# Performance work log

Hardware: AMD Instinct MI355X
Metric: run time of the kernel (lower is better)

The kernel has to match this reference:

```python
import jax, jax.numpy as jnp
import numpy as np

N_HEAD = 16
D_K = 64
D_V = 64
EMBED = 1024
BATCH = 4
SEQ = 2048

def setup_inputs() -> dict:
    key = jax.random.key(0)
    ks = jax.random.split(key, 12)
    s = lambda d: 1.0 / np.sqrt(d)
    u = lambda k, shape, d: jax.random.uniform(k, shape, jnp.float32, -s(d), s(d))
    return {
        'z': jax.random.normal(ks[0], (BATCH, SEQ, EMBED), jnp.float32),
        'wq': u(ks[1], (EMBED, D_K), D_K),
        'wk': u(ks[2], (EMBED, D_K), D_K),
        'wv': u(ks[3], (EMBED, D_V), D_V),
        'fcq_w': u(ks[4], (D_K, N_HEAD * D_K), D_K),
        'fcq_b': u(ks[5], (N_HEAD * D_K,), N_HEAD * D_K),
        'fck_w': u(ks[6], (D_K, N_HEAD * D_K), D_K),
        'fck_b': u(ks[7], (N_HEAD * D_K,), N_HEAD * D_K),
        'fcv_w': u(ks[8], (D_V, N_HEAD * D_V), D_V),
        'fcv_b': u(ks[9], (N_HEAD * D_V,), N_HEAD * D_V),
        'fco_w': u(ks[10], (N_HEAD * D_V, EMBED), EMBED),
        'fco_b': u(ks[11], (EMBED,), EMBED),
    }

def reference(z, wq, wk, wv, fcq_w, fcq_b, fck_w, fck_b, fcv_w, fcv_b, fco_w, fco_b):
    b, n, _ = z.shape
    scale = jnp.sqrt(jnp.float32(D_K))
    # bottleneck projections then per-head expansion
    q = (z @ wq) @ fcq_w + fcq_b  # [b, n, H*dk]
    k = (z @ wk) @ fck_w + fck_b  # [b, n, H*dk]
    v = (z @ wv) @ fcv_w + fcv_b  # [b, n, H*dv]
    q = q.reshape(b, n, N_HEAD, D_K)
    k = k.reshape(b, n, N_HEAD, D_K)
    v = v.reshape(b, n, N_HEAD, D_V)
    scores = jnp.einsum('bihd,bjhd->bhij', q, k) / scale  # [b, H, n, n]
    attn = jax.nn.softmax(scores, axis=-1)
    out = jnp.einsum('bhij,bjhd->bihd', attn, v)  # [b, n, H, dv]
    out = out.reshape(b, n, N_HEAD * D_V)
    return out @ fco_w + fco_b  # [b, n, embed]
```

## Files before the change

kernel.cpp:

```cpp
#include <hip/hip_runtime.h>


typedef __bf16 bf16x8 __attribute__((ext_vector_type(8)));
typedef __bf16 bf16x4 __attribute__((ext_vector_type(4)));
typedef __bf16 bf16x2 __attribute__((ext_vector_type(2)));
typedef float floatx4 __attribute__((ext_vector_type(4)));
typedef float floatx16 __attribute__((ext_vector_type(16)));
typedef unsigned int uintx4 __attribute__((ext_vector_type(4)));
typedef unsigned int uintx2 __attribute__((ext_vector_type(2)));

#define SW64(row, col) (((row) << 6) | (((((col) >> 3) ^ ((row) & 7) ^ (((row) >> 3) & 7)) << 3) | ((col) & 7)))

#if __has_builtin(__builtin_amdgcn_exp2f)
__device__ __forceinline__ float fast_exp2(float x) { return __builtin_amdgcn_exp2f(x); }
#else
__device__ __forceinline__ float fast_exp2(float x) { return exp2f(x); }
#endif

__device__ __forceinline__ unsigned int pack_bf16(float lo, float hi) {
    bf16x2 w; w[0] = (__bf16)lo; w[1] = (__bf16)hi;
    return __builtin_bit_cast(unsigned int, w);
}
__device__ __forceinline__ unsigned int pack2(__bf16 lo, __bf16 hi) {
    bf16x2 w; w[0] = lo; w[1] = hi;
    return __builtin_bit_cast(unsigned int, w);
}
#if __has_builtin(__builtin_amdgcn_permlane32_swap)
__device__ __forceinline__ void xchg(unsigned int& X, unsigned int& Y, int) {
    uintx2 r = __builtin_amdgcn_permlane32_swap(X, Y, false, false);
    X = r[0]; Y = r[1];
}
#else
__device__ __forceinline__ void xchg(unsigned int& X, unsigned int& Y, int hl) {
    unsigned int sX = (unsigned int)__shfl_xor((int)X, 32);
    unsigned int sY = (unsigned int)__shfl_xor((int)Y, 32);
    unsigned int lo = hl ? sY : X;
    unsigned int hi = hl ? Y : sX;
    X = lo; Y = hi;
}
#endif
__device__ __forceinline__ bf16x8 frag4(unsigned int a, unsigned int b, unsigned int c, unsigned int d) {
    uintx4 u; u[0] = a; u[1] = b; u[2] = c; u[3] = d;
    return __builtin_bit_cast(bf16x8, u);
}
__device__ __forceinline__ void async_b128(const __bf16* g, __bf16* l) {
    __builtin_amdgcn_global_load_lds(
        (const __attribute__((address_space(1))) unsigned int*)g,
        (__attribute__((address_space(3))) unsigned int*)l, 16, 0, 0);
}

__device__ __forceinline__ bf16x8 cvt8(const void* src, int f, long idx) {
    bf16x8 v;
    if (f) {
        const float* s = (const float*)src + idx;
        float4 f0 = *(const float4*)s;
        float4 f1 = *(const float4*)(s + 4);
        v[0] = (__bf16)f0.x; v[1] = (__bf16)f0.y; v[2] = (__bf16)f0.z; v[3] = (__bf16)f0.w;
        v[4] = (__bf16)f1.x; v[5] = (__bf16)f1.y; v[6] = (__bf16)f1.z; v[7] = (__bf16)f1.w;
    } else {
        v = *(const bf16x8*)((const __bf16*)src + idx);
    }
    return v;
}

__global__ void detect_dtype(const unsigned short* __restrict__ z, int* __restrict__ flag) {
    __shared__ int cnt;
    if (threadIdx.x == 0) cnt = 0;
    __syncthreads();
    int local = 0;
    for (int i = threadIdx.x; i < 16384; i += 256) {
        unsigned int u = (unsigned int)z[i] << 16;
        float x = __uint_as_float(u);
        float ax = fabsf(x);
        if (!(ax <= 1024.0f) || (x != 0.0f && ax < 1e-20f)) local++;
    }
    atomicAdd(&cnt, local);
    __syncthreads();
    if (threadIdx.x == 0) *flag = (cnt > 1310) ? 1 : 0;
}

struct MegaArgs { const void* z; const void* bias[4]; const void* w[7]; };

__global__ __launch_bounds__(256) void mega_convert(MegaArgs a, __bf16* __restrict__ cv,
                                                    const int* __restrict__ flag) {
    const int f = *flag;
    const unsigned int blk = blockIdx.x;
    const int tid = threadIdx.x;

    if (blk < 1024) {
        const long base = (long)blk * 8192 + tid * 8;
        #pragma unroll
        for (int p = 0; p < 4; p++) {
            const long i = base + p * 2048;
            *(bf16x8*)&cv[i] = cvt8(a.z, f, i);
        }
        return;
    }
    if (blk < 1026) {
        const int idx = (((int)blk - 1024) * 256 + tid) * 8;
        const int b = idx >> 10, o = idx & 1023;
        *(bf16x8*)&cv[9830400 + b * 1024 + o] = cvt8(a.bias[b], f, o);
        return;
    }
    const int t = blk - 1026;
    int bx, by, R, C;
    const void* src;
    __bf16* dst;
    if (t < 48) {
        const int m = t >> 4; by = t & 15; bx = 0; R = 1024; C = 64;
        src = a.w[m]; dst = cv + 8388608 + m * 65536;
    } else if (t < 96) {
        const int m = (t - 48) >> 4; bx = (t - 48) & 15; by = 0; R = 64; C = 1024;
        src = a.w[3 + m]; dst = cv + 8585216 + m * 65536;
    } else {
        const int u = t - 96; bx = u & 15; by = u >> 4; R = 1024; C = 1024;
        src = a.w[6]; dst = cv + 8781824;
    }
    __shared__ __bf16 tl[64][72];
    const int r0 = by * 64, c0 = bx * 64;
    const int rr = tid >> 3, c8 = (tid & 7) << 3;
    #pragma unroll
    for (int p = 0; p < 2; p++) {
        bf16x8 v = cvt8(src, f, (long)(r0 + p * 32 + rr) * C + c0 + c8);
        #pragma unroll
        for (int j = 0; j < 8; j++) tl[c8 + j][p * 32 + rr] = v[j];
    }
    __syncthreads();
    #pragma unroll
    for (int p = 0; p < 2; p++) {
        bf16x8 v;
        #pragma unroll
        for (int j = 0; j < 8; j++) v[j] = tl[p * 32 + rr][c8 + j];
        *(bf16x8*)&dst[(long)(c0 + p * 32 + rr) * R + r0 + c8] = v;
    }
}

__global__ __launch_bounds__(256, 2) void gemm64(
    const __bf16* __restrict__ A,
    const __bf16* __restrict__ BT0, const __bf16* __restrict__ BT1, const __bf16* __restrict__ BT2,
    __bf16* __restrict__ C0, __bf16* __restrict__ C1, __bf16* __restrict__ C2,
    int K)
{
    const int zsel = blockIdx.z;
    const __bf16* BT = (zsel == 0) ? BT0 : (zsel == 1) ? BT1 : BT2;
    __bf16* C = (zsel == 0) ? C0 : (zsel == 1) ? C1 : C2;
    const int m0 = blockIdx.x * 64;
    const int tid = threadIdx.x;
    const int wave = tid >> 6, ln = tid & 63;
    const int l15 = tid & 15, quad = (tid >> 4) & 3;

    __shared__ __bf16 As[64 * 64];
    __shared__ __bf16 Bs[64 * 64];

    const int r_off = ln >> 3, j_off = ln & 7;
    floatx4 acc[4] = {};

    for (int k0 = 0; k0 < K; k0 += 64) {
        __syncthreads();
        #pragma unroll
        for (int it = 0; it < 2; it++) {
            const int seg = wave * 2 + it;
            const int row = seg * 8 + r_off;
            const int c = j_off ^ (row & 7) ^ ((row >> 3) & 7);
            async_b128(&A[(long)(m0 + row) * K + k0 + c * 8], &As[seg * 512]);
            async_b128(&BT[(long)row * K + k0 + c * 8], &Bs[seg * 512]);
        }
        __syncthreads();
        #pragma unroll
        for (int ks = 0; ks < 2; ks++) {
            bf16x8 av = *(const bf16x8*)&As[SW64(wave * 16 + l15, ks * 32 + quad * 8)];
            #pragma unroll
            for (int nt = 0; nt < 4; nt++) {
                bf16x8 bv = *(const bf16x8*)&Bs[SW64(nt * 16 + l15, ks * 32 + quad * 8)];
                acc[nt] = __builtin_amdgcn_mfma_f32_16x16x32_bf16(av, bv, acc[nt], 0, 0, 0);
            }
        }
    }
    #pragma unroll
    for (int nt = 0; nt < 4; nt++) {
        const int col = nt * 16 + l15;
        #pragma unroll
        for (int r = 0; r < 4; r++)
            C[(long)(m0 + wave * 16 + quad * 4 + r) * 64 + col] = (__bf16)acc[nt][r];
    }
}

__global__ __launch_bounds__(256, 2) void gemm128(
    const __bf16* __restrict__ A0, const __bf16* __restrict__ A1, const __bf16* __restrict__ A2,
    const __bf16* __restrict__ BT0, const __bf16* __restrict__ BT1, const __bf16* __restrict__ BT2,
    const __bf16* __restrict__ bias0, const __bf16* __restrict__ bias1, const __bf16* __restrict__ bias2,
    void* __restrict__ C0, void* __restrict__ C1, void* __restrict__ C2,
    int M, int N, int K, const int* flagp,
    float os0, float os1, float os2)
{
    const int zsel = blockIdx.z;
    const __bf16* A = (zsel == 0) ? A0 : (zsel == 1) ? A1 : A2;
    const __bf16* BT = (zsel == 0) ? BT0 : (zsel == 1) ? BT1 : BT2;
    const __bf16* bias = (zsel == 0) ? bias0 : (zsel == 1) ? bias1 : bias2;
    void* C = (zsel == 0) ? C0 : (zsel == 1) ? C1 : C2;
    const float oscale = (zsel == 0) ? os0 : (zsel == 1) ? os1 : os2;
    const int out_fp32 = flagp ? *flagp : 0;

    const int m0 = blockIdx.x * 128;
    const int n0 = blockIdx.y * 128;
    const int tid = threadIdx.x;
    const int wave = tid >> 6, ln = tid & 63;
    const int wr = wave >> 1, wc = wave & 1;
    const int l15 = tid & 15, quad = (tid >> 4) & 3;

    __shared__ __bf16 As[128 * 64];
    __shared__ __bf16 Bs[128 * 64];

    const int r_off = ln >> 3, j_off = ln & 7;

    floatx4 acc[4][4] = {};

    for (int k0 = 0; k0 < K; k0 += 64) {
        __syncthreads();
        #pragma unroll
        for (int it = 0; it < 4; it++) {
            const int seg = wave * 4 + it;
            const int row = seg * 8 + r_off;
            const int c = j_off ^ (row & 7) ^ ((row >> 3) & 7);
            async_b128(&A[(long)(m0 + row) * K + k0 + c * 8], &As[seg * 512]);
            async_b128(&BT[(long)(n0 + row) * K + k0 + c * 8], &Bs[seg * 512]);
        }
        __syncthreads();
        #pragma unroll
        for (int ks = 0; ks < 2; ks++) {
            bf16x8 a[4], b[4];
            #pragma unroll
            for (int rt = 0; rt < 4; rt++)
                a[rt] = *(const bf16x8*)&As[SW64(wr * 64 + rt * 16 + l15, ks * 32 + quad * 8)];
            #pragma unroll
            for (int nt = 0; nt < 4; nt++)
                b[nt] = *(const bf16x8*)&Bs[SW64(wc * 64 + nt * 16 + l15, ks * 32 + quad * 8)];
            #pragma unroll
            for (int rt = 0; rt < 4; rt++)
                #pragma unroll
                for (int nt = 0; nt < 4; nt++)
                    acc[rt][nt] = __builtin_amdgcn_mfma_f32_16x16x32_bf16(a[rt], b[nt], acc[rt][nt], 0, 0, 0);
        }
    }
    #pragma unroll
    for (int rt = 0; rt < 4; rt++) {
        const int row = m0 + wr * 64 + rt * 16 + quad * 4;
        #pragma unroll
        for (int nt = 0; nt < 4; nt++) {
            const int col = n0 + wc * 64 + nt * 16 + l15;
            float bv = (float)bias[col];
            #pragma unroll
            for (int r = 0; r < 4; r++) {
                float val = (acc[rt][nt][r] + bv) * oscale;
                if (out_fp32) ((float*)C)[(long)(row + r) * N + col] = val;
                else ((__bf16*)C)[(long)(row + r) * N + col] = (__bf16)val;
            }
        }
    }
}

__global__ __launch_bounds__(256, 3) void attn_kernel(
    const __bf16* __restrict__ Qg, const __bf16* __restrict__ Kg,
    const __bf16* __restrict__ Vg, __bf16* __restrict__ Og)
{
    const int bh = blockIdx.x;
    const int b = bh >> 4, h = bh & 15;
    const int q0 = blockIdx.y * 128;
    const int base = b * 2048 * 1024 + h * 64;
    const int tid = threadIdx.x;
    const int wave = tid >> 6, ln = tid & 63;
    const int l31 = ln & 31, hl = ln >> 5;
    const int h8 = hl * 8;

    __shared__ __bf16 Ks[2][64 * 64];
    __shared__ __bf16 VTs[2][64 * 64];

    bf16x8 qf[4];
    #pragma unroll
    for (int ks = 0; ks < 4; ks++)
        qf[ks] = *(const bf16x8*)&Qg[base + (q0 + wave * 32 + l31) * 1024 + ks * 16 + h8];

    const int kr = tid >> 3, kc = (tid & 7) << 3;
    const int vr2 = (tid >> 3) * 2, vc = (tid & 7) << 3;

    {
        bf16x8 ka = *(const bf16x8*)&Kg[base + kr * 1024 + kc];
        bf16x8 kb = *(const bf16x8*)&Kg[base + (kr + 32) * 1024 + kc];
        bf16x8 va = *(const bf16x8*)&Vg[base + vr2 * 1024 + vc];
        bf16x8 vb = *(const bf16x8*)&Vg[base + (vr2 + 1) * 1024 + vc];
        *(bf16x8*)&Ks[0][SW64(kr, kc)] = ka;
        *(bf16x8*)&Ks[0][SW64(kr + 32, kc)] = kb;
        #pragma unroll
        for (int j = 0; j < 8; j++)
            *(unsigned int*)&VTs[0][SW64(vc + j, vr2)] = pack2(va[j], vb[j]);
    }

    floatx16 o_acc[2] = {};
    float m_i = -1e30f, l_i = 0.0f;

    for (int t = 0; t < 32; t++) {
        const int cur = t & 1, nxt = cur ^ 1;
        bf16x8 nka, nkb, nva, nvb;
        if (t < 31) {
            const int kvn = (t + 1) * 64;
            nka = *(const bf16x8*)&Kg[base + (kvn + kr) * 1024 + kc];
            nkb = *(const bf16x8*)&Kg[base + (kvn + kr + 32) * 1024 + kc];
            nva = *(const bf16x8*)&Vg[base + (kvn + vr2) * 1024 + vc];
            nvb = *(const bf16x8*)&Vg[base + (kvn + vr2 + 1) * 1024 + vc];
        }
        __syncthreads();

        floatx16 sv[2] = {};
        #pragma unroll
        for (int ks = 0; ks < 4; ks++) {
            bf16x8 a0 = *(const bf16x8*)&Ks[cur][SW64(l31, ks * 16 + h8)];
            bf16x8 a1 = *(const bf16x8*)&Ks[cur][SW64(32 + l31, ks * 16 + h8)];
            sv[0] = __builtin_amdgcn_mfma_f32_32x32x16_bf16(a0, qf[ks], sv[0], 0, 0, 0);
            sv[1] = __builtin_amdgcn_mfma_f32_32x32x16_bf16(a1, qf[ks], sv[1], 0, 0, 0);
        }

        float m8[8];
        #pragma unroll
        for (int r = 0; r < 8; r++)
            m8[r] = fmaxf(fmaxf(fmaxf(sv[0][r], sv[0][r + 8]), sv[1][r]), sv[1][r + 8]);
        float ma = fmaxf(fmaxf(m8[0], m8[1]), m8[2]);
        float mb = fmaxf(fmaxf(m8[3], m8[4]), m8[5]);
        float mc = fmaxf(fmaxf(m8[6], m8[7]), ma);
        float mx = fmaxf(mb, mc);
        mx = fmaxf(mx, __shfl_xor(mx, 32));

        if (__any(mx > m_i + 8.0f)) {
            float m_new = fmaxf(m_i, mx);
            float alpha = fast_exp2(m_i - m_new);
            m_i = m_new;
            l_i *= alpha;
            #pragma unroll
            for (int dt = 0; dt < 2; dt++)
                #pragma unroll
                for (int r = 0; r < 16; r++) o_acc[dt][r] *= alpha;
        }

        float rsA = 0.f, rsB = 0.f, rsC = 0.f, rsD = 0.f;
        bf16x8 pf0, pf1, pf2, pf3;
        #define PGROUP(SVV, BASE, PF) { \
            float e0 = fast_exp2(SVV[BASE + 0] - m_i), e1 = fast_exp2(SVV[BASE + 1] - m_i); \
            float e2 = fast_exp2(SVV[BASE + 2] - m_i), e3 = fast_exp2(SVV[BASE + 3] - m_i); \
            float e4 = fast_exp2(SVV[BASE + 4] - m_i), e5 = fast_exp2(SVV[BASE + 5] - m_i); \
            float e6 = fast_exp2(SVV[BASE + 6] - m_i), e7 = fast_exp2(SVV[BASE + 7] - m_i); \
            rsA += e0 + e4; rsB += e1 + e5; rsC += e2 + e6; rsD += e3 + e7; \
            unsigned int Aw = pack_bf16(e0, e1), Bw = pack_bf16(e2, e3); \
            unsigned int Cw = pack_bf16(e4, e5), Dw = pack_bf16(e6, e7); \
            xchg(Aw, Cw, hl); xchg(Bw, Dw, hl); \
            PF = frag4(Aw, Bw, Cw, Dw); }
        PGROUP(sv[0], 0, pf0)
        PGROUP(sv[0], 8, pf1)
        PGROUP(sv[1], 0, pf2)
        PGROUP(sv[1], 8, pf3)
        #undef PGROUP
        float rs = (rsA + rsB) + (rsC + rsD);
        rs += __shfl_xor(rs, 32);
        l_i += rs;

        if (t < 31) {
            *(bf16x8*)&Ks[nxt][SW64(kr, kc)] = nka;
            *(bf16x8*)&Ks[nxt][SW64(kr + 32, kc)] = nkb;
        }

        #pragma unroll
        for (int js = 0; js < 4; js++) {
            bf16x8 av0 = *(const bf16x8*)&VTs[cur][SW64(l31, js * 16 + h8)];
            bf16x8 av1 = *(const bf16x8*)&VTs[cur][SW64(32 + l31, js * 16 + h8)];
            bf16x8 pb = (js == 0) ? pf0 : (js == 1) ? pf1 : (js == 2) ? pf2 : pf3;
            o_acc[0] = __builtin_amdgcn_mfma_f32_32x32x16_bf16(av0, pb, o_acc[0], 0, 0, 0);
            o_acc[1] = __builtin_amdgcn_mfma_f32_32x32x16_bf16(av1, pb, o_acc[1], 0, 0, 0);
        }

        if (t < 31) {
            #pragma unroll
            for (int j = 0; j < 8; j++)
                *(unsigned int*)&VTs[nxt][SW64(vc + j, vr2)] = pack2(nva[j], nvb[j]);
        }
    }

    float inv = 1.0f / l_i;
    const int orow = q0 + wave * 32 + l31;
    #pragma unroll
    for (int dt = 0; dt < 2; dt++)
        #pragma unroll
        for (int g = 0; g < 4; g++) {
            bf16x4 ov;
            #pragma unroll
            for (int e = 0; e < 4; e++) ov[e] = (__bf16)(o_acc[dt][g * 4 + e] * inv);
            *(bf16x4*)&Og[base + orow * 1024 + dt * 32 + g * 8 + hl * 4] = ov;
        }
}

extern "C" void kernel_launch(void* const* d_in, const int* in_sizes, int n_in,
                              void* d_out, int out_size, void* d_ws, size_t ws_size,
                              hipStream_t stream)
{
    int* flag = (int*)d_ws;
    __bf16* cv = (__bf16*)((char*)d_ws + 256);

    const int Z = 0, WQT = 8388608, FCWT = 8585216, FCOWT = 8781824, BIAS = 9830400;
    __bf16* zb = cv + 10485760;
    __bf16* Qw = cv + 12582912;
    __bf16* Kw = Qw + 8388608;
    __bf16* Vw = Kw + 8388608;
    __bf16* Ow = cv + Z;

    detect_dtype<<<1, 256, 0, stream>>>((const unsigned short*)d_in[0], flag);

    MegaArgs ma;
    ma.z = d_in[0];
    ma.bias[0] = d_in[5]; ma.bias[1] = d_in[7]; ma.bias[2] = d_in[9]; ma.bias[3] = d_in[11];
    ma.w[0] = d_in[1]; ma.w[1] = d_in[2]; ma.w[2] = d_in[3];
    ma.w[3] = d_in[4]; ma.w[4] = d_in[6]; ma.w[5] = d_in[8];
    ma.w[6] = d_in[10];
    mega_convert<<<dim3(1378, 1), 256, 0, stream>>>(ma, cv, flag);

    gemm64<<<dim3(128, 1, 3), 256, 0, stream>>>(
        cv + Z, cv + WQT, cv + WQT + 65536, cv + WQT + 131072,
        zb, zb + 524288, zb + 1048576, 1024);

    const float QSC = 0.125f * 1.44269504088896f;
    gemm128<<<dim3(64, 8, 3), 256, 0, stream>>>(
        zb, zb + 524288, zb + 1048576,
        cv + FCWT, cv + FCWT + 65536, cv + FCWT + 131072,
        cv + BIAS, cv + BIAS + 1024, cv + BIAS + 2048,
        Qw, Kw, Vw, 8192, 1024, 64, nullptr,
        QSC, 1.0f, 1.0f);

    attn_kernel<<<dim3(64, 16), 256, 0, stream>>>(Qw, Kw, Vw, Ow);

    gemm128<<<dim3(64, 8, 1), 256, 0, stream>>>(
        Ow, Ow, Ow, cv + FCOWT, cv + FCOWT, cv + FCOWT,
        cv + BIAS + 3072, cv + BIAS + 3072, cv + BIAS + 3072,
        d_out, d_out, d_out, 8192, 1024, 1024, flag,
        1.0f, 1.0f, 1.0f);
}
```

Measured before the change: 267.5 us.

## Fuse bottleneck and head-expansion GEMMs; compute softmax row sums via MFMA

New measurement: 274.6 us. 2.6% more time.

```diff
diff --git a/kernel.cpp b/kernel.cpp
--- a/kernel.cpp
+++ b/kernel.cpp
@@ -135,15 +135,21 @@
     }
 }
 
-__global__ __launch_bounds__(256, 2) void gemm64(
+__global__ __launch_bounds__(256, 2) void gemm_qkv(
     const __bf16* __restrict__ A,
-    const __bf16* __restrict__ BT0, const __bf16* __restrict__ BT1, const __bf16* __restrict__ BT2,
-    __bf16* __restrict__ C0, __bf16* __restrict__ C1, __bf16* __restrict__ C2,
-    int K)
+    const __bf16* __restrict__ W1T,
+    const __bf16* __restrict__ W2T,
+    const __bf16* __restrict__ biases,
+    __bf16* __restrict__ Q0, __bf16* __restrict__ Q1, __bf16* __restrict__ Q2,
+    float os0)
 {
     const int zsel = blockIdx.z;
-    const __bf16* BT = (zsel == 0) ? BT0 : (zsel == 1) ? BT1 : BT2;
-    __bf16* C = (zsel == 0) ? C0 : (zsel == 1) ? C1 : C2;
+    const __bf16* BT1 = W1T + zsel * 65536;
+    const __bf16* BT2 = W2T + zsel * 65536;
+    const __bf16* bias = biases + zsel * 1024;
+    __bf16* Q = (zsel == 0) ? Q0 : (zsel == 1) ? Q1 : Q2;
+    const float oscale = (zsel == 0) ? os0 : 1.0f;
+
     const int m0 = blockIdx.x * 64;
     const int tid = threadIdx.x;
     const int wave = tid >> 6, ln = tid & 63;
@@ -151,19 +157,21 @@
 
     __shared__ __bf16 As[64 * 64];
     __shared__ __bf16 Bs[64 * 64];
+    __shared__ __bf16 Zs[64 * 64];
+    __shared__ __bf16 Ws[128 * 64];
 
     const int r_off = ln >> 3, j_off = ln & 7;
     floatx4 acc[4] = {};
 
-    for (int k0 = 0; k0 < K; k0 += 64) {
+    for (int k0 = 0; k0 < 1024; k0 += 64) {
         __syncthreads();
         #pragma unroll
         for (int it = 0; it < 2; it++) {
             const int seg = wave * 2 + it;
             const int row = seg * 8 + r_off;
             const int c = j_off ^ (row & 7) ^ ((row >> 3) & 7);
-            async_b128(&A[(long)(m0 + row) * K + k0 + c * 8], &As[seg * 512]);
-            async_b128(&BT[(long)row * K + k0 + c * 8], &Bs[seg * 512]);
+            async_b128(&A[(long)(m0 + row) * 1024 + k0 + c * 8], &As[seg * 512]);
+            async_b128(&BT1[(long)row * 1024 + k0 + c * 8], &Bs[seg * 512]);
         }
         __syncthreads();
         #pragma unroll
@@ -181,26 +189,46 @@
         const int col = nt * 16 + l15;
         #pragma unroll
         for (int r = 0; r < 4; r++)
-            C[(long)(m0 + wave * 16 + quad * 4 + r) * 64 + col] = (__bf16)acc[nt][r];
+            Zs[SW64(wave * 16 + quad * 4 + r, col)] = (__bf16)acc[nt][r];
+    }
+    for (int nc = 0; nc < 8; nc++) {
+        __syncthreads();
+        #pragma unroll
+        for (int it = 0; it < 4; it++) {
+            const int seg = wave * 4 + it;
+            const int row = seg * 8 + r_off;
+            const int c = j_off ^ (row & 7) ^ ((row >> 3) & 7);
+            async_b128(&BT2[(long)(nc * 128 + row) * 64 + c * 8], &Ws[seg * 512]);
+        }
+        __syncthreads();
+        floatx4 acc2[8] = {};
+        #pragma unroll
+        for (int ks = 0; ks < 2; ks++) {
+            bf16x8 av = *(const bf16x8*)&Zs[SW64(wave * 16 + l15, ks * 32 + quad * 8)];
+            #pragma unroll
+            for (int nt = 0; nt < 8; nt++) {
+                bf16x8 bv = *(const bf16x8*)&Ws[SW64(nt * 16 + l15, ks * 32 + quad * 8)];
+                acc2[nt] = __builtin_amdgcn_mfma_f32_16x16x32_bf16(av, bv, acc2[nt], 0, 0, 0);
+            }
+        }
+        #pragma unroll
+        for (int nt = 0; nt < 8; nt++) {
+            const int col = nc * 128 + nt * 16 + l15;
+            float bv = (float)bias[col];
+            #pragma unroll
+            for (int r = 0; r < 4; r++)
+                Q[(long)(m0 + wave * 16 + quad * 4 + r) * 1024 + col] =
+                    (__bf16)((acc2[nt][r] + bv) * oscale);
+        }
     }
 }
 
 __global__ __launch_bounds__(256, 2) void gemm128(
-    const __bf16* __restrict__ A0, const __bf16* __restrict__ A1, const __bf16* __restrict__ A2,
-    const __bf16* __restrict__ BT0, const __bf16* __restrict__ BT1, const __bf16* __restrict__ BT2,
-    const __bf16* __restrict__ bias0, const __bf16* __restrict__ bias1, const __bf16* __restrict__ bias2,
-    void* __restrict__ C0, void* __restrict__ C1, void* __restrict__ C2,
-    int M, int N, int K, const int* flagp,
-    float os0, float os1, float os2)
+    const __bf16* __restrict__ A, const __bf16* __restrict__ BT,
+    const __bf16* __restrict__ bias, void* __restrict__ C,
+    int M, int N, int K, const int* flagp, float oscale)
 {
-    const int zsel = blockIdx.z;
-    const __bf16* A = (zsel == 0) ? A0 : (zsel == 1) ? A1 : A2;
-    const __bf16* BT = (zsel == 0) ? BT0 : (zsel == 1) ? BT1 : BT2;
-    const __bf16* bias = (zsel == 0) ? bias0 : (zsel == 1) ? bias1 : bias2;
-    void* C = (zsel == 0) ? C0 : (zsel == 1) ? C1 : C2;
-    const float oscale = (zsel == 0) ? os0 : (zsel == 1) ? os1 : os2;
     const int out_fp32 = flagp ? *flagp : 0;
-
     const int m0 = blockIdx.x * 128;
     const int n0 = blockIdx.y * 128;
     const int tid = threadIdx.x;
@@ -280,6 +308,13 @@
     for (int ks = 0; ks < 4; ks++)
         qf[ks] = *(const bf16x8*)&Qg[base + (q0 + wave * 32 + l31) * 1024 + ks * 16 + h8];
 
+    bf16x8 onesf;
+    {
+        __bf16 v = (l31 == 0) ? (__bf16)1.0f : (__bf16)0.0f;
+        #pragma unroll
+        for (int e = 0; e < 8; e++) onesf[e] = v;
+    }
+
     const int kr = tid >> 3, kc = (tid & 7) << 3;
     const int vr2 = (tid >> 3) * 2, vc = (tid & 7) << 3;
 
@@ -296,7 +331,8 @@
     }
 
     floatx16 o_acc[2] = {};
-    float m_i = -1e30f, l_i = 0.0f;
+    floatx16 lsum = {};
+    float m_i = -1e30f;
 
     for (int t = 0; t < 32; t++) {
         const int cur = t & 1, nxt = cur ^ 1;
@@ -333,21 +369,19 @@
             float m_new = fmaxf(m_i, mx);
             float alpha = fast_exp2(m_i - m_new);
             m_i = m_new;
-            l_i *= alpha;
+            lsum[0] *= alpha;
             #pragma unroll
             for (int dt = 0; dt < 2; dt++)
                 #pragma unroll
                 for (int r = 0; r < 16; r++) o_acc[dt][r] *= alpha;
         }
 
-        float rsA = 0.f, rsB = 0.f, rsC = 0.f, rsD = 0.f;
         bf16x8 pf0, pf1, pf2, pf3;
         #define PGROUP(SVV, BASE, PF) { \
             float e0 = fast_exp2(SVV[BASE + 0] - m_i), e1 = fast_exp2(SVV[BASE + 1] - m_i); \
             float e2 = fast_exp2(SVV[BASE + 2] - m_i), e3 = fast_exp2(SVV[BASE + 3] - m_i); \
             float e4 = fast_exp2(SVV[BASE + 4] - m_i), e5 = fast_exp2(SVV[BASE + 5] - m_i); \
             float e6 = fast_exp2(SVV[BASE + 6] - m_i), e7 = fast_exp2(SVV[BASE + 7] - m_i); \
-            rsA += e0 + e4; rsB += e1 + e5; rsC += e2 + e6; rsD += e3 + e7; \
             unsigned int Aw = pack_bf16(e0, e1), Bw = pack_bf16(e2, e3); \
             unsigned int Cw = pack_bf16(e4, e5), Dw = pack_bf16(e6, e7); \
             xchg(Aw, Cw, hl); xchg(Bw, Dw, hl); \
@@ -357,9 +391,6 @@
         PGROUP(sv[1], 0, pf2)
         PGROUP(sv[1], 8, pf3)
         #undef PGROUP
-        float rs = (rsA + rsB) + (rsC + rsD);
-        rs += __shfl_xor(rs, 32);
-        l_i += rs;
 
         if (t < 31) {
             *(bf16x8*)&Ks[nxt][SW64(kr, kc)] = nka;
@@ -373,6 +404,7 @@
             bf16x8 pb = (js == 0) ? pf0 : (js == 1) ? pf1 : (js == 2) ? pf2 : pf3;
             o_acc[0] = __builtin_amdgcn_mfma_f32_32x32x16_bf16(av0, pb, o_acc[0], 0, 0, 0);
             o_acc[1] = __builtin_amdgcn_mfma_f32_32x32x16_bf16(av1, pb, o_acc[1], 0, 0, 0);
+            lsum = __builtin_amdgcn_mfma_f32_32x32x16_bf16(onesf, pb, lsum, 0, 0, 0);
         }
 
         if (t < 31) {
@@ -382,7 +414,9 @@
         }
     }
 
-    float inv = 1.0f / l_i;
+    float lv = lsum[0];
+    lv += __shfl_xor(lv, 32);
+    float inv = 1.0f / lv;
     const int orow = q0 + wave * 32 + l31;
     #pragma unroll
     for (int dt = 0; dt < 2; dt++)
@@ -403,7 +437,6 @@
     __bf16* cv = (__bf16*)((char*)d_ws + 256);
 
     const int Z = 0, WQT = 8388608, FCWT = 8585216, FCOWT = 8781824, BIAS = 9830400;
-    __bf16* zb = cv + 10485760;
     __bf16* Qw = cv + 12582912;
     __bf16* Kw = Qw + 8388608;
     __bf16* Vw = Kw + 8388608;
@@ -419,23 +452,14 @@
     ma.w[6] = d_in[10];
     mega_convert<<<dim3(1378, 1), 256, 0, stream>>>(ma, cv, flag);
 
-    gemm64<<<dim3(128, 1, 3), 256, 0, stream>>>(
-        cv + Z, cv + WQT, cv + WQT + 65536, cv + WQT + 131072,
-        zb, zb + 524288, zb + 1048576, 1024);
-
     const float QSC = 0.125f * 1.44269504088896f;
-    gemm128<<<dim3(64, 8, 3), 256, 0, stream>>>(
-        zb, zb + 524288, zb + 1048576,
-        cv + FCWT, cv + FCWT + 65536, cv + FCWT + 131072,
-        cv + BIAS, cv + BIAS + 1024, cv + BIAS + 2048,
-        Qw, Kw, Vw, 8192, 1024, 64, nullptr,
-        QSC, 1.0f, 1.0f);
+    gemm_qkv<<<dim3(128, 1, 3), 256, 0, stream>>>(
+        cv + Z, cv + WQT, cv + FCWT, cv + BIAS,
+        Qw, Kw, Vw, QSC);
 
     attn_kernel<<<dim3(64, 16), 256, 0, stream>>>(Qw, Kw, Vw, Ow);
 
     gemm128<<<dim3(64, 8, 1), 256, 0, stream>>>(
-        Ow, Ow, Ow, cv + FCOWT, cv + FCOWT, cv + FCOWT,
-        cv + BIAS + 3072, cv + BIAS + 3072, cv + BIAS + 3072,
-        d_out, d_out, d_out, 8192, 1024, 1024, flag,
-        1.0f, 1.0f, 1.0f);
-}
+        Ow, cv + FCOWT, cv + BIAS + 3072,
+        d_out, 8192, 1024, 1024, flag, 1.0f);
+}
```
